# Kernel tuning notes

Measured on AMD Instinct MI355X. Metric: run time of the kernel, lower is better.

The kernel has to match this reference:

```python
import jax, jax.numpy as jnp
import numpy as np

N_NODES = 100000
N_EDGES = 1600000
IN_DIM, HID_DIM, OUT_DIM = 128, 128, 64


def setup_inputs() -> dict:
    key = jax.random.key(0)
    k1, k2, k3, k4, k5, k6, k7 = jax.random.split(key, 7)
    in_feat = jax.random.normal(k1, (N_NODES, IN_DIM), dtype=jnp.float32)
    src = jax.random.randint(k2, (N_EDGES,), 0, N_NODES, dtype=jnp.int32)
    dst = jax.random.randint(k3, (N_EDGES,), 0, N_NODES, dtype=jnp.int32)
    # GraphConv params (Glorot-style scale)
    W1 = jax.random.normal(k4, (IN_DIM, HID_DIM), dtype=jnp.float32) * (2.0 / (IN_DIM + HID_DIM)) ** 0.5
    b1 = jnp.zeros((HID_DIM,), dtype=jnp.float32)
    W2 = jax.random.normal(k5, (HID_DIM, OUT_DIM), dtype=jnp.float32) * (2.0 / (HID_DIM + OUT_DIM)) ** 0.5
    b2 = jnp.zeros((OUT_DIM,), dtype=jnp.float32)
    return {"in_feat": in_feat, "W1": W1, "b1": b1, "W2": W2, "b2": b2, "src": src, "dst": dst}


def _graph_conv(x, W, b, src, dst, inv_sqrt_out, inv_sqrt_in):
    # DGL GraphConv, norm='both': D_out^{-1/2} on source, sum-aggregate, D_in^{-1/2} on dest
    x = x * inv_sqrt_out[:, None]              # [N, d]
    msg = x[src]                               # gather: [E, d]
    agg = jax.ops.segment_sum(msg, dst, num_segments=x.shape[0])  # scatter-add: [N, d]
    agg = agg * inv_sqrt_in[:, None]
    return agg @ W + b


def reference(in_feat, W1, b1, W2, b2, src, dst):
    N = in_feat.shape[0]
    ones = jnp.ones(src.shape[0], dtype=in_feat.dtype)
    deg_out = jax.ops.segment_sum(ones, src, num_segments=N)
    deg_in = jax.ops.segment_sum(ones, dst, num_segments=N)
    # clamp degree to >= 1 (DGL behavior) before inverse sqrt
    inv_sqrt_out = jnp.maximum(deg_out, 1.0) ** -0.5
    inv_sqrt_in = jnp.maximum(deg_in, 1.0) ** -0.5
    h = _graph_conv(in_feat, W1, b1, src, dst, inv_sqrt_out, inv_sqrt_in)
    h = jax.nn.relu(h)
    h = _graph_conv(h, W2, b2, src, dst, inv_sqrt_out, inv_sqrt_in)
    return h
```

## Files before the change

### kernel.cpp

```cpp
#include <hip/hip_runtime.h>

#define N_NODES 100000
#define N_EDGES 1600000
#define IN_DIM 128
#define HID_DIM 128
#define OUT_DIM 64

#define NB 391
#define GRIDB 256
#define EPB (N_EDGES / GRIDB)
#define CELLS (NB * GRIDB)
#define SNPART (CELLS / 256)

typedef unsigned short ushort_t;
typedef unsigned int uint_t;
typedef __attribute__((ext_vector_type(8))) short bf16x8;
typedef __attribute__((ext_vector_type(4))) float f32x4;

__device__ __forceinline__ float blo(uint_t u) { return __uint_as_float(u << 16); }
__device__ __forceinline__ float bhi(uint_t u) { return __uint_as_float(u & 0xFFFF0000u); }
__device__ __forceinline__ uint_t f2b(float f) {
    uint_t u = __float_as_uint(f);
    uint_t r = u + 0x7FFFu + ((u >> 16) & 1u);
    return r >> 16;
}
__device__ __forceinline__ uint_t pk2(float a, float b) { return f2b(a) | (f2b(b) << 16); }


__global__ __launch_bounds__(256) void histdeg_k(const int* __restrict__ src,
                                                 const int* __restrict__ dst,
                                                 int* __restrict__ dego,
                                                 int* __restrict__ hist) {
    __shared__ int h[NB];
    int t = threadIdx.x, blk = blockIdx.x;
    for (int j = t; j < NB; j += 256) h[j] = 0;
    __syncthreads();
    int e0 = blk * EPB;
    for (int i = e0 + t; i < e0 + EPB; i += 256) {
        atomicAdd(&h[dst[i] >> 8], 1);
        atomicAdd(&dego[src[i]], 1);
    }
    __syncthreads();
    for (int j = t; j < NB; j += 256) hist[j * GRIDB + blk] = h[j];
}


__global__ __launch_bounds__(256) void scan_part_k(const int* __restrict__ in,
                                                   int* __restrict__ partial, int L) {
    __shared__ int s[256];
    int t = threadIdx.x, i = blockIdx.x * 256 + t;
    s[t] = (i < L) ? in[i] : 0;
    __syncthreads();
    for (int off = 128; off > 0; off >>= 1) {
        if (t < off) s[t] += s[t + off];
        __syncthreads();
    }
    if (t == 0) partial[blockIdx.x] = s[0];
}

__global__ __launch_bounds__(512) void scan_top_k(const int* __restrict__ partial,
                                                  int* __restrict__ partofs, int n) {
    __shared__ int s[512];
    int t = threadIdx.x;
    int v = (t < n) ? partial[t] : 0;
    s[t] = v;
    __syncthreads();
    for (int off = 1; off < 512; off <<= 1) {
        int x = (t >= off) ? s[t - off] : 0;
        __syncthreads();
        s[t] += x;
        __syncthreads();
    }
    if (t < n) partofs[t] = s[t] - v;
}

__global__ __launch_bounds__(256) void scan_final_k(const int* __restrict__ in,
                                                    const int* __restrict__ partofs,
                                                    int* __restrict__ out, int L) {
    __shared__ int s[256];
    int t = threadIdx.x, i = blockIdx.x * 256 + t;
    int v = (i < L) ? in[i] : 0;
    s[t] = v;
    __syncthreads();
    for (int off = 1; off < 256; off <<= 1) {
        int x = (t >= off) ? s[t - off] : 0;
        __syncthreads();
        s[t] += x;
        __syncthreads();
    }
    if (i < L) out[i] = partofs[blockIdx.x] + s[t] - v;
}


__global__ __launch_bounds__(256) void scat_k(const int* __restrict__ src,
                                              const int* __restrict__ dst,
                                              const int* __restrict__ histOfs,
                                              uint_t* __restrict__ ebuf) {
    __shared__ int base[NB];
    __shared__ int lcnt[NB];
    int t = threadIdx.x, blk = blockIdx.x;
    for (int j = t; j < NB; j += 256) {
        base[j] = histOfs[j * GRIDB + blk];
        lcnt[j] = 0;
    }
    __syncthreads();
    int e0 = blk * EPB;
    for (int i = e0 + t; i < e0 + EPB; i += 256) {
        int d = dst[i];
        int b = d >> 8;
        int slot = atomicAdd(&lcnt[b], 1);
        ebuf[base[b] + slot] = (uint_t)src[i] | ((uint_t)(d & 255) << 17);
    }
}


__global__ __launch_bounds__(256) void fin_k(const uint_t* __restrict__ ebuf,
                                             const int* __restrict__ histOfs,
                                             int* __restrict__ ofs,
                                             int* __restrict__ esrc) {
    __shared__ int cnt[256];
    __shared__ int s[256];
    __shared__ int fil[256];
    int b = blockIdx.x, t = threadIdx.x;
    int e0 = histOfs[b * GRIDB];
    int e1 = (b == NB - 1) ? N_EDGES : histOfs[(b + 1) * GRIDB];
    cnt[t] = 0;
    __syncthreads();
    for (int i = e0 + t; i < e1; i += 256) atomicAdd(&cnt[ebuf[i] >> 17], 1);
    __syncthreads();
    int c = cnt[t];
    s[t] = c;
    __syncthreads();
    for (int off = 1; off < 256; off <<= 1) {
        int x = (t >= off) ? s[t - off] : 0;
        __syncthreads();
        s[t] += x;
        __syncthreads();
    }
    int excl = s[t] - c;
    int node = b * 256 + t;
    if (node < N_NODES) ofs[node] = e0 + excl;
    if (b == NB - 1 && t == 0) ofs[N_NODES] = N_EDGES;
    fil[t] = excl;
    __syncthreads();
    for (int i = e0 + t; i < e1; i += 256) {
        uint_t u = ebuf[i];
        int slot = atomicAdd(&fil[u >> 17], 1);
        esrc[e0 + slot] = (int)(u & 0x1FFFFu);
    }
}


__global__ __launch_bounds__(256) void prep_k(const float* __restrict__ x,
                                              const int* __restrict__ dego,
                                              ushort_t* __restrict__ xs) {
    int gid = blockIdx.x * 256 + threadIdx.x;
    int row = gid >> 4;
    float s = rsqrtf(fmaxf((float)dego[row], 1.0f));
    const float4* xp = (const float4*)x + (size_t)gid * 2;
    float4 va = xp[0], vb = xp[1];
    ((uint4*)xs)[gid] = make_uint4(pk2(va.x * s, va.y * s), pk2(va.z * s, va.w * s),
                                   pk2(vb.x * s, vb.y * s), pk2(vb.z * s, vb.w * s));
}


__global__ __launch_bounds__(256) void wprep2_k(const float* __restrict__ W1,
                                                const float* __restrict__ W2,
                                                ushort_t* __restrict__ Wf1,
                                                ushort_t* __restrict__ Wf2) {
    int gid = blockIdx.x * 256 + threadIdx.x;
    const float* W;
    ushort_t* Wf;
    int BN;
    if (gid < HID_DIM * 16) {
        W = W1; Wf = Wf1; BN = HID_DIM;
    } else {
        gid -= HID_DIM * 16;
        if (gid >= OUT_DIM * 16) return;
        W = W2; Wf = Wf2; BN = OUT_DIM;
    }
    int l = gid & 63;
    int kc = (gid >> 6) & 3;
    int nt = gid >> 8;
    int col = nt * 16 + (l & 15);
    int k0 = kc * 32 + (l >> 4) * 8;
    uint_t r[4];
    #pragma unroll
    for (int p = 0; p < 4; ++p)
        r[p] = pk2(W[(size_t)(k0 + 2 * p) * BN + col], W[(size_t)(k0 + 2 * p + 1) * BN + col]);
    ((uint4*)Wf)[gid] = make_uint4(r[0], r[1], r[2], r[3]);
}

#define ACC8(v)                                         \
    acc[0] += blo(v.x); acc[1] += bhi(v.x);             \
    acc[2] += blo(v.y); acc[3] += bhi(v.y);             \
    acc[4] += blo(v.z); acc[5] += bhi(v.z);             \
    acc[6] += blo(v.w); acc[7] += bhi(v.w);


__global__ __launch_bounds__(256) void agg128_k(const ushort_t* __restrict__ xs,
                                                const int* __restrict__ esrc,
                                                const int* __restrict__ ofs,
                                                ushort_t* __restrict__ a) {
    int wid = (blockIdx.x * 256 + threadIdx.x) >> 6;
    int lane = threadIdx.x & 63;
    int q = lane >> 4, li = lane & 15;
    int beg = ofs[wid], end = ofs[wid + 1];
    float acc[8];
    #pragma unroll
    for (int i = 0; i < 8; ++i) acc[i] = 0.f;

    for (int j = beg; j < end; j += 64) {
        int m = end - j;
        if (m > 64) m = 64;
        int idx = (lane < m) ? esrc[j + lane] : 0;
        for (int t = 0; 4 * t < m; t += 4) {
            int e0 = 4 * t + q, e1 = e0 + 4, e2 = e0 + 8, e3 = e0 + 12;
            int s0 = __shfl(idx, e0 & 63);
            int s1 = __shfl(idx, e1 & 63);
            int s2 = __shfl(idx, e2 & 63);
            int s3 = __shfl(idx, e3 & 63);
            uint4 v0 = *(const uint4*)(xs + (size_t)s0 * 128 + li * 8);
            uint4 v1 = *(const uint4*)(xs + (size_t)s1 * 128 + li * 8);
            uint4 v2 = *(const uint4*)(xs + (size_t)s2 * 128 + li * 8);
            uint4 v3 = *(const uint4*)(xs + (size_t)s3 * 128 + li * 8);
            if (e0 < m) { ACC8(v0) }
            if (e1 < m) { ACC8(v1) }
            if (e2 < m) { ACC8(v2) }
            if (e3 < m) { ACC8(v3) }
        }
    }
    #pragma unroll
    for (int i = 0; i < 8; ++i) acc[i] += __shfl(acc[i], lane ^ 16);
    #pragma unroll
    for (int i = 0; i < 8; ++i) acc[i] += __shfl(acc[i], lane ^ 32);

    if (lane < 16) {
        float sc = rsqrtf(fmaxf((float)(end - beg), 1.0f));
        *(uint4*)(a + (size_t)wid * 128 + li * 8) =
            make_uint4(pk2(acc[0] * sc, acc[1] * sc), pk2(acc[2] * sc, acc[3] * sc),
                       pk2(acc[4] * sc, acc[5] * sc), pk2(acc[6] * sc, acc[7] * sc));
    }
}


__global__ __launch_bounds__(256) void mgemm12_k(const ushort_t* __restrict__ A,
                                                 const ushort_t* __restrict__ Wf1,
                                                 const ushort_t* __restrict__ Wf2,
                                                 const float* __restrict__ b1,
                                                 const int* __restrict__ dego,
                                                 ushort_t* __restrict__ ys) {
    __shared__ ushort_t Hs[4][16][136];
    int wv = threadIdx.x >> 6;
    int l = threadIdx.x & 63;
    int r0 = (blockIdx.x * 4 + wv) * 16;
    if (r0 >= N_NODES) return;
    int q = l >> 4, li = l & 15;

    const ushort_t* ap = A + (size_t)(r0 + li) * 128 + q * 8;
    bf16x8 af[4];
    #pragma unroll
    for (int kc = 0; kc < 4; ++kc) af[kc] = *(const bf16x8*)(ap + kc * 32);

    f32x4 acc[8];
    #pragma unroll
    for (int nt = 0; nt < 8; ++nt) acc[nt] = (f32x4){0.f, 0.f, 0.f, 0.f};

    #pragma unroll
    for (int kc = 0; kc < 4; ++kc) {
        #pragma unroll
        for (int nt = 0; nt < 8; ++nt) {
            bf16x8 bfr = *(const bf16x8*)(Wf1 + ((size_t)(nt * 4 + kc) * 64 + l) * 8);
            acc[nt] = __builtin_amdgcn_mfma_f32_16x16x32_bf16(af[kc], bfr, acc[nt], 0, 0, 0);
        }
    }

    #pragma unroll
    for (int nt = 0; nt < 8; ++nt) {
        float bv = b1[nt * 16 + li];
        #pragma unroll
        for (int j = 0; j < 4; ++j) {
            float x = fmaxf(acc[nt][j] + bv, 0.0f);
            Hs[wv][q * 4 + j][nt * 16 + li] = (ushort_t)f2b(x);
        }
    }

    bf16x8 hf[4];
    #pragma unroll
    for (int kc = 0; kc < 4; ++kc)
        hf[kc] = *(const bf16x8*)&Hs[wv][li][kc * 32 + q * 8];

    f32x4 acc2[4];
    #pragma unroll
    for (int nt = 0; nt < 4; ++nt) acc2[nt] = (f32x4){0.f, 0.f, 0.f, 0.f};

    #pragma unroll
    for (int kc = 0; kc < 4; ++kc) {
        #pragma unroll
        for (int nt = 0; nt < 4; ++nt) {
            bf16x8 bfr = *(const bf16x8*)(Wf2 + ((size_t)(nt * 4 + kc) * 64 + l) * 8);
            acc2[nt] = __builtin_amdgcn_mfma_f32_16x16x32_bf16(hf[kc], bfr, acc2[nt], 0, 0, 0);
        }
    }

    int orow = r0 + q * 4;
    float os[4];
    #pragma unroll
    for (int j = 0; j < 4; ++j) os[j] = rsqrtf(fmaxf((float)dego[orow + j], 1.0f));
    #pragma unroll
    for (int nt = 0; nt < 4; ++nt) {
        #pragma unroll
        for (int j = 0; j < 4; ++j) {
            ys[(size_t)(orow + j) * 64 + nt * 16 + li] = (ushort_t)f2b(acc2[nt][j] * os[j]);
        }
    }
}


__global__ __launch_bounds__(256) void agg64_k(const ushort_t* __restrict__ ys,
                                               const int* __restrict__ esrc,
                                               const int* __restrict__ ofs,
                                               const float* __restrict__ b2,
                                               float* __restrict__ out) {
    int wid = (blockIdx.x * 256 + threadIdx.x) >> 6;
    int lane = threadIdx.x & 63;
    int og = lane >> 3, li = lane & 7;
    int beg = ofs[wid], end = ofs[wid + 1];
    float acc[8];
    #pragma unroll
    for (int i = 0; i < 8; ++i) acc[i] = 0.f;

    for (int j = beg; j < end; j += 64) {
        int m = end - j;
        if (m > 64) m = 64;
        int idx = (lane < m) ? esrc[j + lane] : 0;
        for (int t = 0; 8 * t < m; t += 2) {
            int e0 = 8 * t + og, e1 = e0 + 8;
            int s0 = __shfl(idx, e0 & 63);
            int s1 = __shfl(idx, e1 & 63);
            uint4 v0 = *(const uint4*)(ys + (size_t)s0 * 64 + li * 8);
            uint4 v1 = *(const uint4*)(ys + (size_t)s1 * 64 + li * 8);
            if (e0 < m) { ACC8(v0) }
            if (e1 < m) { ACC8(v1) }
        }
    }
    #pragma unroll
    for (int i = 0; i < 8; ++i) acc[i] += __shfl(acc[i], lane ^ 8);
    #pragma unroll
    for (int i = 0; i < 8; ++i) acc[i] += __shfl(acc[i], lane ^ 16);
    #pragma unroll
    for (int i = 0; i < 8; ++i) acc[i] += __shfl(acc[i], lane ^ 32);

    if (lane < 8) {
        float sc = rsqrtf(fmaxf((float)(end - beg), 1.0f));
        float4 ba = *(const float4*)(b2 + li * 8);
        float4 bb = *(const float4*)(b2 + li * 8 + 4);
        float* op = out + (size_t)wid * 64 + li * 8;
        *(float4*)op = make_float4(acc[0] * sc + ba.x, acc[1] * sc + ba.y,
                                   acc[2] * sc + ba.z, acc[3] * sc + ba.w);
        *(float4*)(op + 4) = make_float4(acc[4] * sc + bb.x, acc[5] * sc + bb.y,
                                         acc[6] * sc + bb.z, acc[7] * sc + bb.w);
    }
}

extern "C" void kernel_launch(void* const* d_in, const int* in_sizes, int n_in,
                              void* d_out, int out_size, void* d_ws, size_t ws_size,
                              hipStream_t stream) {
    const float* in_feat = (const float*)d_in[0];
    const float* W1 = (const float*)d_in[1];
    const float* b1 = (const float*)d_in[2];
    const float* W2 = (const float*)d_in[3];
    const float* b2 = (const float*)d_in[4];
    const int* src = (const int*)d_in[5];
    const int* dst = (const int*)d_in[6];
    float* out = (float*)d_out;

    char* w = (char*)d_ws;
    int* dego = (int*)w;       w += (size_t)N_NODES * 4;
    int* ofs = (int*)w;        w += (size_t)(N_NODES + 4) * 4;
    int* hist = (int*)w;       w += (size_t)CELLS * 4;
    int* histOfs = (int*)w;    w += (size_t)CELLS * 4;
    int* partial = (int*)w;    w += 512 * 4;
    int* partofs = (int*)w;    w += 512 * 4;
    uint_t* ebuf = (uint_t*)w; w += (size_t)N_EDGES * 4;
    int* esrc = (int*)w;       w += (size_t)N_EDGES * 4;
    ushort_t* Wf1 = (ushort_t*)w; w += (size_t)HID_DIM * 16 * 16;
    ushort_t* Wf2 = (ushort_t*)w; w += (size_t)OUT_DIM * 16 * 16;
    ushort_t* bufA = (ushort_t*)w; w += (size_t)N_NODES * HID_DIM * 2;
    ushort_t* bufB = (ushort_t*)w; w += (size_t)N_NODES * HID_DIM * 2;

    hipMemsetAsync(dego, 0, (size_t)N_NODES * 4, stream);
    histdeg_k<<<GRIDB, 256, 0, stream>>>(src, dst, dego, hist);

    scan_part_k<<<SNPART, 256, 0, stream>>>(hist, partial, CELLS);
    scan_top_k<<<1, 512, 0, stream>>>(partial, partofs, SNPART);
    scan_final_k<<<SNPART, 256, 0, stream>>>(hist, partofs, histOfs, CELLS);

    scat_k<<<GRIDB, 256, 0, stream>>>(src, dst, histOfs, ebuf);
    fin_k<<<NB, 256, 0, stream>>>(ebuf, histOfs, ofs, esrc);

    wprep2_k<<<(HID_DIM * 16 + OUT_DIM * 16 + 255) / 256, 256, 0, stream>>>(W1, W2, Wf1, Wf2);

    prep_k<<<N_NODES * 16 / 256, 256, 0, stream>>>(in_feat, dego, bufA);
    agg128_k<<<N_NODES / 4, 256, 0, stream>>>(bufA, esrc, ofs, bufB);

    mgemm12_k<<<(N_NODES / 16 + 3) / 4, 256, 0, stream>>>(bufB, Wf1, Wf2, b1, dego, bufA);

    agg64_k<<<N_NODES / 4, 256, 0, stream>>>(bufA, esrc, ofs, b2, out);
}
```

Measured before the change: 272.7 us.

## Replace per-block histogram scan with global bucket atomics and merge prep kernels

```diff
diff --git a/kernel.cpp b/kernel.cpp
--- a/kernel.cpp
+++ b/kernel.cpp
@@ -9,8 +9,6 @@
 #define NB 391
 #define GRIDB 256
 #define EPB (N_EDGES / GRIDB)
-#define CELLS (NB * GRIDB)
-#define SNPART (CELLS / 256)
 
 typedef unsigned short ushort_t;
 typedef unsigned int uint_t;
@@ -30,7 +28,7 @@
 __global__ __launch_bounds__(256) void histdeg_k(const int* __restrict__ src,
                                                  const int* __restrict__ dst,
                                                  int* __restrict__ dego,
-                                                 int* __restrict__ hist) {
+                                                 int* __restrict__ bucketTot) {
     __shared__ int h[NB];
     int t = threadIdx.x, blk = blockIdx.x;
     for (int j = t; j < NB; j += 256) h[j] = 0;
@@ -41,28 +39,17 @@
         atomicAdd(&dego[src[i]], 1);
     }
     __syncthreads();
-    for (int j = t; j < NB; j += 256) hist[j * GRIDB + blk] = h[j];
-}
-
-
-__global__ __launch_bounds__(256) void scan_part_k(const int* __restrict__ in,
-                                                   int* __restrict__ partial, int L) {
-    __shared__ int s[256];
-    int t = threadIdx.x, i = blockIdx.x * 256 + t;
-    s[t] = (i < L) ? in[i] : 0;
-    __syncthreads();
-    for (int off = 128; off > 0; off >>= 1) {
-        if (t < off) s[t] += s[t + off];
-        __syncthreads();
-    }
-    if (t == 0) partial[blockIdx.x] = s[0];
-}
-
-__global__ __launch_bounds__(512) void scan_top_k(const int* __restrict__ partial,
-                                                  int* __restrict__ partofs, int n) {
+    for (int j = t; j < NB; j += 256)
+        if (h[j]) atomicAdd(&bucketTot[j], h[j]);
+}
+
+
+__global__ __launch_bounds__(512) void bscan_k(const int* __restrict__ bucketTot,
+                                               int* __restrict__ bucketOfs,
+                                               int* __restrict__ fill) {
     __shared__ int s[512];
     int t = threadIdx.x;
-    int v = (t < n) ? partial[t] : 0;
+    int v = (t < NB) ? bucketTot[t] : 0;
     s[t] = v;
     __syncthreads();
     for (int off = 1; off < 512; off <<= 1) {
@@ -71,59 +58,55 @@
         s[t] += x;
         __syncthreads();
     }
-    if (t < n) partofs[t] = s[t] - v;
-}
-
-__global__ __launch_bounds__(256) void scan_final_k(const int* __restrict__ in,
-                                                    const int* __restrict__ partofs,
-                                                    int* __restrict__ out, int L) {
-    __shared__ int s[256];
-    int t = threadIdx.x, i = blockIdx.x * 256 + t;
-    int v = (i < L) ? in[i] : 0;
-    s[t] = v;
-    __syncthreads();
-    for (int off = 1; off < 256; off <<= 1) {
-        int x = (t >= off) ? s[t - off] : 0;
-        __syncthreads();
-        s[t] += x;
-        __syncthreads();
-    }
-    if (i < L) out[i] = partofs[blockIdx.x] + s[t] - v;
+    if (t < NB) {
+        int e = s[t] - v;
+        bucketOfs[t] = e;
+        fill[t] = e;
+    }
+    if (t == 0) bucketOfs[NB] = N_EDGES;
 }
 
 
 __global__ __launch_bounds__(256) void scat_k(const int* __restrict__ src,
                                               const int* __restrict__ dst,
-                                              const int* __restrict__ histOfs,
+                                              int* __restrict__ fill,
                                               uint_t* __restrict__ ebuf) {
+    __shared__ int lcnt[NB];
     __shared__ int base[NB];
-    __shared__ int lcnt[NB];
+    __shared__ int lpos[NB];
     int t = threadIdx.x, blk = blockIdx.x;
     for (int j = t; j < NB; j += 256) {
-        base[j] = histOfs[j * GRIDB + blk];
         lcnt[j] = 0;
+        lpos[j] = 0;
     }
     __syncthreads();
     int e0 = blk * EPB;
+    for (int i = e0 + t; i < e0 + EPB; i += 256) atomicAdd(&lcnt[dst[i] >> 8], 1);
+    __syncthreads();
+    for (int j = t; j < NB; j += 256) {
+        int c = lcnt[j];
+        base[j] = c ? atomicAdd(&fill[j], c) : 0;
+    }
+    __syncthreads();
     for (int i = e0 + t; i < e0 + EPB; i += 256) {
         int d = dst[i];
         int b = d >> 8;
-        int slot = atomicAdd(&lcnt[b], 1);
+        int slot = atomicAdd(&lpos[b], 1);
         ebuf[base[b] + slot] = (uint_t)src[i] | ((uint_t)(d & 255) << 17);
     }
 }
 
 
 __global__ __launch_bounds__(256) void fin_k(const uint_t* __restrict__ ebuf,
-                                             const int* __restrict__ histOfs,
+                                             const int* __restrict__ bucketOfs,
                                              int* __restrict__ ofs,
                                              int* __restrict__ esrc) {
     __shared__ int cnt[256];
     __shared__ int s[256];
     __shared__ int fil[256];
     int b = blockIdx.x, t = threadIdx.x;
-    int e0 = histOfs[b * GRIDB];
-    int e1 = (b == NB - 1) ? N_EDGES : histOfs[(b + 1) * GRIDB];
+    int e0 = bucketOfs[b];
+    int e1 = bucketOfs[b + 1];
     cnt[t] = 0;
     __syncthreads();
     for (int i = e0 + t; i < e1; i += 256) atomicAdd(&cnt[ebuf[i] >> 17], 1);
@@ -151,24 +134,25 @@
 }
 
 
-__global__ __launch_bounds__(256) void prep_k(const float* __restrict__ x,
-                                              const int* __restrict__ dego,
-                                              ushort_t* __restrict__ xs) {
-    int gid = blockIdx.x * 256 + threadIdx.x;
-    int row = gid >> 4;
-    float s = rsqrtf(fmaxf((float)dego[row], 1.0f));
-    const float4* xp = (const float4*)x + (size_t)gid * 2;
-    float4 va = xp[0], vb = xp[1];
-    ((uint4*)xs)[gid] = make_uint4(pk2(va.x * s, va.y * s), pk2(va.z * s, va.w * s),
-                                   pk2(vb.x * s, vb.y * s), pk2(vb.z * s, vb.w * s));
-}
-
-
-__global__ __launch_bounds__(256) void wprep2_k(const float* __restrict__ W1,
-                                                const float* __restrict__ W2,
-                                                ushort_t* __restrict__ Wf1,
-                                                ushort_t* __restrict__ Wf2) {
-    int gid = blockIdx.x * 256 + threadIdx.x;
+__global__ __launch_bounds__(256) void prepw_k(const float* __restrict__ x,
+                                               const int* __restrict__ dego,
+                                               ushort_t* __restrict__ xs,
+                                               const float* __restrict__ W1,
+                                               const float* __restrict__ W2,
+                                               ushort_t* __restrict__ Wf1,
+                                               ushort_t* __restrict__ Wf2) {
+    constexpr int NB_PREP = N_NODES * 16 / 256;
+    if ((int)blockIdx.x < NB_PREP) {
+        int gid = blockIdx.x * 256 + threadIdx.x;
+        int row = gid >> 4;
+        float s = rsqrtf(fmaxf((float)dego[row], 1.0f));
+        const float4* xp = (const float4*)x + (size_t)gid * 2;
+        float4 va = xp[0], vb = xp[1];
+        ((uint4*)xs)[gid] = make_uint4(pk2(va.x * s, va.y * s), pk2(va.z * s, va.w * s),
+                                       pk2(vb.x * s, vb.y * s), pk2(vb.z * s, vb.w * s));
+        return;
+    }
+    int gid = (blockIdx.x - NB_PREP) * 256 + threadIdx.x;
     const float* W;
     ushort_t* Wf;
     int BN;
@@ -377,11 +361,10 @@
 
     char* w = (char*)d_ws;
     int* dego = (int*)w;       w += (size_t)N_NODES * 4;
+    int* bucketTot = (int*)w;  w += 392 * 4;
+    int* fill = (int*)w;       w += 392 * 4;
+    int* bucketOfs = (int*)w;  w += 400 * 4;
     int* ofs = (int*)w;        w += (size_t)(N_NODES + 4) * 4;
-    int* hist = (int*)w;       w += (size_t)CELLS * 4;
-    int* histOfs = (int*)w;    w += (size_t)CELLS * 4;
-    int* partial = (int*)w;    w += 512 * 4;
-    int* partofs = (int*)w;    w += 512 * 4;
     uint_t* ebuf = (uint_t*)w; w += (size_t)N_EDGES * 4;
     int* esrc = (int*)w;       w += (size_t)N_EDGES * 4;
     ushort_t* Wf1 = (ushort_t*)w; w += (size_t)HID_DIM * 16 * 16;
@@ -389,19 +372,15 @@
     ushort_t* bufA = (ushort_t*)w; w += (size_t)N_NODES * HID_DIM * 2;
     ushort_t* bufB = (ushort_t*)w; w += (size_t)N_NODES * HID_DIM * 2;
 
-    hipMemsetAsync(dego, 0, (size_t)N_NODES * 4, stream);
-    histdeg_k<<<GRIDB, 256, 0, stream>>>(src, dst, dego, hist);
-
-    scan_part_k<<<SNPART, 256, 0, stream>>>(hist, partial, CELLS);
-    scan_top_k<<<1, 512, 0, stream>>>(partial, partofs, SNPART);
-    scan_final_k<<<SNPART, 256, 0, stream>>>(hist, partofs, histOfs, CELLS);
-
-    scat_k<<<GRIDB, 256, 0, stream>>>(src, dst, histOfs, ebuf);
-    fin_k<<<NB, 256, 0, stream>>>(ebuf, histOfs, ofs, esrc);
-
-    wprep2_k<<<(HID_DIM * 16 + OUT_DIM * 16 + 255) / 256, 256, 0, stream>>>(W1, W2, Wf1, Wf2);
-
-    prep_k<<<N_NODES * 16 / 256, 256, 0, stream>>>(in_feat, dego, bufA);
+    hipMemsetAsync(dego, 0, (size_t)(N_NODES + 392) * 4, stream);
+
+    histdeg_k<<<GRIDB, 256, 0, stream>>>(src, dst, dego, bucketTot);
+    bscan_k<<<1, 512, 0, stream>>>(bucketTot, bucketOfs, fill);
+    scat_k<<<GRIDB, 256, 0, stream>>>(src, dst, fill, ebuf);
+    fin_k<<<NB, 256, 0, stream>>>(ebuf, bucketOfs, ofs, esrc);
+
+    prepw_k<<<N_NODES * 16 / 256 + 12, 256, 0, stream>>>(in_feat, dego, bufA, W1, W2, Wf1, Wf2);
+
     agg128_k<<<N_NODES / 4, 256, 0, stream>>>(bufA, esrc, ofs, bufB);
 
     mgemm12_k<<<(N_NODES / 16 + 3) / 4, 256, 0, stream>>>(bufB, Wf1, Wf2, b1, dego, bufA);
```

Result: no change. 274.6 us (+0.7%).
